# Optimization experiments

Hardware: AMD Instinct MI355X
Metric: run time of the kernel (lower is better)

Reference implementation:

```python
import jax, jax.numpy as jnp
import numpy as np

HEADS = 8
CONTEXT_FRAMES = 128
REL_POS_MAX = 128


def setup_inputs() -> dict:
    key = jax.random.key(0)
    ks = jax.random.split(key, 6)
    b, c, f, t = 2, 512, 64, 512
    x = jax.random.normal(ks[0], (b, c, f, t), dtype=jnp.float32)
    # Linear weights stored as [in, out] (equivalent to torch weight.T)
    W_qkv = jax.random.normal(ks[1], (c, 3 * c), dtype=jnp.float32) * (c ** -0.5)
    b_qkv = jnp.zeros((3 * c,), dtype=jnp.float32)
    W_proj = jax.random.normal(ks[2], (c, c), dtype=jnp.float32) * (c ** -0.5)
    b_proj = jnp.zeros((c,), dtype=jnp.float32)
    rel_pos_bias = jax.random.normal(ks[3], (HEADS, REL_POS_MAX), dtype=jnp.float32) * 0.02
    return {"x": x, "W_qkv": W_qkv, "b_qkv": b_qkv, "W_proj": W_proj,
            "b_proj": b_proj, "rel_pos_bias": rel_pos_bias}


def reference(x, W_qkv, b_qkv, W_proj, b_proj, rel_pos_bias):
    b, c, f, t = x.shape
    hd = c // HEADS
    # (b, c, f, t) -> (b*f, t, c)
    h = jnp.transpose(x, (0, 2, 3, 1)).reshape(b * f, t, c)
    qkv = (h @ W_qkv + b_qkv).reshape(b * f, t, 3, HEADS, hd)
    q, k, v = qkv[:, :, 0], qkv[:, :, 1], qkv[:, :, 2]  # [bf, t, H, hd]
    scale = hd ** -0.5
    scores = jnp.einsum('nqhd,nkhd->nhqk', q, k) * scale  # [bf, H, t, t]
    # causal band mask + gathered relative-position bias
    dist = jnp.arange(t)[:, None] - jnp.arange(t)[None, :]  # [t, t]
    invalid = (dist < 0) | (dist >= CONTEXT_FRAMES)
    bias = rel_pos_bias[:, jnp.clip(dist, 0, REL_POS_MAX - 1)]  # [H, t, t]
    scores = scores + bias[None]
    scores = jnp.where(invalid[None, None], -jnp.inf, scores)
    attn = jax.nn.softmax(scores, axis=-1)
    y = jnp.einsum('nhqk,nkhd->nqhd', attn, v).reshape(b * f, t, c)
    y = y @ W_proj + b_proj
    return jnp.transpose(y.reshape(b, f, t, c), (0, 3, 1, 2))
```

## Files before the change

kernel.cpp:

```cpp
#include <hip/hip_runtime.h>
#include <hip/hip_bf16.h>

typedef short s16x8 __attribute__((ext_vector_type(8)));
typedef unsigned short u16x4 __attribute__((ext_vector_type(4)));
typedef float f32x4 __attribute__((ext_vector_type(4)));

#define MFMA16(a,b,c) __builtin_amdgcn_mfma_f32_16x16x32_bf16((a),(b),(c),0,0,0)

__device__ __forceinline__ unsigned short f2bf(float x){
  unsigned int u = __float_as_uint(x);
  u += 0x7fffu + ((u >> 16) & 1u);
  return (unsigned short)(u >> 16);
}

__device__ __forceinline__ void gl_lds16(const unsigned short* g, unsigned short* l){
  __builtin_amdgcn_global_load_lds((const __attribute__((address_space(1))) unsigned int*)g,
                                   (__attribute__((address_space(3))) unsigned int*)l, 16, 0, 0);
}

__global__ void __launch_bounds__(256) wt_prep(const float* __restrict__ Wq, const float* __restrict__ Wp,
                                               unsigned short* __restrict__ WqT, unsigned short* __restrict__ WpT){
  __shared__ unsigned short tb[64][65];
  int blk = blockIdx.x;
  const float* src; unsigned short* dst; int N, k0, n0;
  if (blk < 192){
    src = Wq; dst = WqT; N = 1536;
    n0 = (blk % 24)*64; k0 = (blk / 24)*64;
  } else {
    blk -= 192; src = Wp; dst = WpT; N = 512;
    n0 = (blk & 7)*64; k0 = (blk >> 3)*64;
  }
  const int tid = threadIdx.x;
  const int nl = tid & 63;
  #pragma unroll
  for (int it = 0; it < 16; ++it){
    const int kl = it*4 + (tid >> 6);
    tb[kl][nl] = f2bf(src[(size_t)(k0+kl)*N + n0 + nl]);
  }
  __syncthreads();
  const int c2 = (tid & 31)*2;
  #pragma unroll
  for (int it = 0; it < 8; ++it){
    const int nw = it*8 + (tid >> 5);
    unsigned int v = (unsigned int)tb[c2][nw] | ((unsigned int)tb[c2+1][nw] << 16);
    *(unsigned int*)(dst + (size_t)(n0+nw)*512 + k0 + c2) = v;
  }
}

__global__ void __launch_bounds__(256) x_to_h(const float* __restrict__ x, unsigned short* __restrict__ h){
  __shared__ unsigned short tb[64][65];
  const int blk = blockIdx.x;
  const int ttt = blk & 7, cht = (blk >> 3) & 7, n = blk >> 6;
  const int b = n >> 6, f = n & 63;
  const int t = threadIdx.x;
  const int tt0 = ttt*64, ch0 = cht*64;
  const float* xb = x + ((size_t)(b*512 + ch0)*64 + f)*512 + tt0;
  const int ttl = t & 63;
  #pragma unroll
  for (int it = 0; it < 16; ++it){
    const int chl = it*4 + (t >> 6);
    tb[chl][ttl] = f2bf(xb[(size_t)chl*32768 + ttl]);
  }
  __syncthreads();
  unsigned short* hb = h + ((size_t)n*512 + tt0)*512 + ch0;
  const int c2 = (t & 31)*2;
  #pragma unroll
  for (int it = 0; it < 8; ++it){
    const int ttw = it*8 + (t >> 5);
    unsigned int v = (unsigned int)tb[c2][ttw] | ((unsigned int)tb[c2+1][ttw] << 16);
    *(unsigned int*)(hb + (size_t)ttw*512 + c2) = v;
  }
}

__device__ __forceinline__ void gemm_core_128(const unsigned short* __restrict__ A,
                                              const unsigned short* __restrict__ Bt,
                                              char* smem, int bm, int bn, int tid,
                                              f32x4 (&acc)[4][4]){
  const int lane = tid & 63, w = tid >> 6;
  const int wr = w >> 1, wc = w & 1;
  const int glog = (lane & 7) ^ ((lane >> 3) & 7);
  const unsigned short* Ab = A  + (size_t)(bm*128 + w*32 + (lane>>3))*512 + glog*8;
  const unsigned short* Bb = Bt + (size_t)(bn*128 + w*32 + (lane>>3))*512 + glog*8;
  unsigned short* AsW = (unsigned short*)smem + w*2048;
  unsigned short* BsW = (unsigned short*)(smem + 16384) + w*2048;
  const int rowoff = (lane & 15)*128;
  const int axor = lane & 7;
  const int ag = lane >> 4;
  for (int kt = 0; kt < 8; ++kt){
    const unsigned short* Ag = Ab + kt*64;
    const unsigned short* Bg = Bb + kt*64;
    gl_lds16(Ag          , AsW);
    gl_lds16(Ag +  8*512 , AsW + 512);
    gl_lds16(Ag + 16*512 , AsW + 1024);
    gl_lds16(Ag + 24*512 , AsW + 1536);
    gl_lds16(Bg          , BsW);
    gl_lds16(Bg +  8*512 , BsW + 512);
    gl_lds16(Bg + 16*512 , BsW + 1024);
    gl_lds16(Bg + 24*512 , BsW + 1536);
    __syncthreads();
    #pragma unroll
    for (int ks = 0; ks < 2; ++ks){
      s16x8 av[4], bv[4];
      const int g16 = ((ks*4 + ag) ^ axor) * 16;
      #pragma unroll
      for (int i = 0; i < 4; ++i){
        av[i] = *(const s16x8*)(smem +         (wr*64 + i*16)*128 + rowoff + g16);
        bv[i] = *(const s16x8*)(smem + 16384 + (wc*64 + i*16)*128 + rowoff + g16);
      }
      #pragma unroll
      for (int i = 0; i < 4; ++i)
        #pragma unroll
        for (int j = 0; j < 4; ++j)
          acc[i][j] = MFMA16(av[i], bv[j], acc[i][j]);
    }
    __syncthreads();
  }
}

__global__ void __launch_bounds__(256) qkv_gemm(const unsigned short* __restrict__ h,
                                                const unsigned short* __restrict__ WqT,
                                                const float* __restrict__ bqkv,
                                                unsigned short* __restrict__ Qb,
                                                unsigned short* __restrict__ Kb,
                                                unsigned short* __restrict__ Vt){
  __shared__ __align__(16) char smem[34816];
  const int tid = threadIdx.x;
  const int bm = blockIdx.x / 12, bn = blockIdx.x % 12;
  f32x4 acc[4][4] = {};
  gemm_core_128(h, WqT, smem, bm, bn, tid, acc);
  const int lane = tid & 63, w = tid >> 6, wr = w >> 1, wc = w & 1;
  const int c0 = bn * 128;
  float bj[4];
  #pragma unroll
  for (int j = 0; j < 4; ++j) bj[j] = bqkv[c0 + wc*64 + j*16 + (lane & 15)];
  unsigned short* Cs = (unsigned short*)smem;
  #pragma unroll
  for (int i = 0; i < 4; ++i)
    #pragma unroll
    for (int j = 0; j < 4; ++j)
      #pragma unroll
      for (int r = 0; r < 4; ++r){
        const int row = wr*64 + i*16 + (lane>>4)*4 + r;
        const int col = wc*64 + j*16 + (lane & 15);
        Cs[row*136 + col] = f2bf(acc[i][j][r] + bj[j]);
      }
  __syncthreads();
  const int n = bm >> 2, tt0 = (bm & 3) * 128;
  const int sel = bn >> 2, cq0 = (bn & 3) * 128;
  if (sel < 2){
    unsigned short* dst = (sel == 0) ? Qb : Kb;
    #pragma unroll
    for (int it = 0; it < 8; ++it){
      const int idx = it*256 + tid;
      const int row = idx >> 4, colc = (idx & 15)*8;
      const int cq = cq0 + colc, head = cq >> 6, d0 = cq & 63;
      s16x8 v = *(const s16x8*)(Cs + row*136 + colc);
      *(s16x8*)(dst + ((size_t)(n*8 + head)*512 + tt0 + row)*64 + d0) = v;
    }
  } else {
    const int col = tid >> 1;
    const int cq = cq0 + col, head = cq >> 6, d = cq & 63;
    #pragma unroll
    for (int it = 0; it < 8; ++it){
      const int ttl0 = (it*2 + (tid & 1))*8;
      s16x8 v;
      #pragma unroll
      for (int r = 0; r < 8; ++r) v[r] = (short)Cs[(ttl0 + r)*136 + col];
      *(s16x8*)(Vt + ((size_t)(n*8 + head)*64 + d)*512 + tt0 + ttl0) = v;
    }
  }
}

__global__ void __launch_bounds__(256) attn_kernel(const unsigned short* __restrict__ Qb,
                                                   const unsigned short* __restrict__ Kb,
                                                   const unsigned short* __restrict__ Vt,
                                                   const float* __restrict__ relb,
                                                   unsigned short* __restrict__ ys){
  __shared__ __align__(16) unsigned short KsL[2][4096];
  __shared__ __align__(16) unsigned short VsL[2][4096];
  __shared__ __align__(16) unsigned short P[4][2][16*72];
  __shared__ float biasS[128];
  const int blk = blockIdx.x;
  const int qt = blk & 3, hh = (blk >> 2) & 7, n = blk >> 5;
  const int tid = threadIdx.x, lane = tid & 63, w = tid >> 6;
  if (tid < 128) biasS[tid] = relb[hh*128 + tid];
  const int q0 = qt * 128;
  const size_t nh = (size_t)(n*8 + hh);
  const unsigned short* Kbase = Kb + nh*32768;
  const unsigned short* Vbase = Vt + nh*32768;
  const int lq = lane & 15, lg = lane >> 4;
  const int qq0 = q0 + w*32;
  s16x8 bq[2][2];
  #pragma unroll
  for (int qs = 0; qs < 2; ++qs){
    const unsigned short* Qp = Qb + (nh*512 + qq0 + qs*16 + lq)*64 + lg*8;
    bq[qs][0] = *(const s16x8*)(Qp);
    bq[qs][1] = *(const s16x8*)(Qp + 32);
  }
  int r_[2], g_[2], dsl_[2];
  #pragma unroll
  for (int j = 0; j < 2; ++j){
    const int slot = j*256 + w*64 + lane;
    r_[j] = slot >> 3;
    g_[j] = (slot & 7) ^ (r_[j] & 7);
    dsl_[j] = (j*256 + w*64) * 8;
  }
  f32x4 yacc[2][4] = {{{0.f,0.f,0.f,0.f}}};
  float m_run[2] = {-INFINITY, -INFINITY}, l_run[2] = {0.f, 0.f};
  const int first = (q0 >= 128) ? 0 : ((128 - q0 + 63) >> 6);
  int cur = 0;
  {
    const int kt0 = q0 - 128 + first*64;
    #pragma unroll
    for (int j = 0; j < 2; ++j){
      gl_lds16(Kbase + (size_t)(kt0 + r_[j])*64 + g_[j]*8, KsL[0] + dsl_[j]);
      gl_lds16(Vbase + (size_t)r_[j]*512 + kt0 + g_[j]*8,  VsL[0] + dsl_[j]);
    }
  }
  for (int kt = first; kt < 4; ++kt){
    const int kt0 = q0 - 128 + kt*64;
    __syncthreads();
    if (kt < 3){
      const int nk0 = kt0 + 64;
      #pragma unroll
      for (int j = 0; j < 2; ++j){
        gl_lds16(Kbase + (size_t)(nk0 + r_[j])*64 + g_[j]*8, KsL[cur^1] + dsl_[j]);
        gl_lds16(Vbase + (size_t)r_[j]*512 + nk0 + g_[j]*8,  VsL[cur^1] + dsl_[j]);
      }
    }
    const bool wact = (kt0 <= qq0 + 31);
    if (wact){
      s16x8 av[4][2];
      #pragma unroll
      for (int mk = 0; mk < 4; ++mk){
        const int rr = mk*16 + lq;
        const unsigned short* kp = KsL[cur] + rr*64;
        av[mk][0] = *(const s16x8*)(kp + ((lg     ) ^ (rr & 7))*8);
        av[mk][1] = *(const s16x8*)(kp + ((4 + lg ) ^ (rr & 7))*8);
      }
      float pex[2][4][4];
      #pragma unroll
      for (int qs = 0; qs < 2; ++qs){
        const int qqs = qq0 + qs*16;
        if (kt0 > qqs + 15 || kt0 + 63 < qqs - 127) continue;
        f32x4 s4[4] = {{0.f,0.f,0.f,0.f}};
        #pragma unroll
        for (int mk = 0; mk < 4; ++mk){
          s4[mk] = MFMA16(av[mk][0], bq[qs][0], s4[mk]);
          s4[mk] = MFMA16(av[mk][1], bq[qs][1], s4[mk]);
        }
        const int qg = qqs + lq;
        float pmax = -3.0e38f;
        #pragma unroll
        for (int mk = 0; mk < 4; ++mk)
          #pragma unroll
          for (int r = 0; r < 4; ++r){
            const int dist = qg - (kt0 + mk*16 + lg*4 + r);
            float xv;
            if (dist >= 0 && dist < 128) xv = s4[mk][r]*0.125f + biasS[dist];
            else                         xv = -1.0e30f;
            pex[qs][mk][r] = xv;
            pmax = fmaxf(pmax, xv);
          }
        pmax = fmaxf(pmax, __shfl_xor(pmax, 16, 64));
        pmax = fmaxf(pmax, __shfl_xor(pmax, 32, 64));
        const float m_new = fmaxf(m_run[qs], pmax);
        const float scalef = __expf(m_run[qs] - m_new);
        float psum = 0.f;
        unsigned short* Pw = P[w][qs];
        #pragma unroll
        for (int mk = 0; mk < 4; ++mk){
          u16x4 pk;
          #pragma unroll
          for (int r = 0; r < 4; ++r){
            const float pe = __expf(pex[qs][mk][r] - m_new);
            psum += pe;
            pk[r] = f2bf(pe);
          }
          *(u16x4*)(Pw + lq*72 + mk*16 + lg*4) = pk;
        }
        psum += __shfl_xor(psum, 16, 64);
        psum += __shfl_xor(psum, 32, 64);
        l_run[qs] = l_run[qs]*scalef + psum;
        m_run[qs] = m_new;
        #pragma unroll
        for (int i = 0; i < 4; ++i) yacc[qs][i] *= scalef;
      }
      s16x8 vv[4][2];
      #pragma unroll
      for (int i = 0; i < 4; ++i){
        const int rr = i*16 + lq;
        const unsigned short* vp = VsL[cur] + rr*64;
        vv[i][0] = *(const s16x8*)(vp + ((lg    ) ^ (rr & 7))*8);
        vv[i][1] = *(const s16x8*)(vp + ((4 + lg) ^ (rr & 7))*8);
      }
      #pragma unroll
      for (int qs = 0; qs < 2; ++qs){
        const int qqs = qq0 + qs*16;
        if (kt0 > qqs + 15 || kt0 + 63 < qqs - 127) continue;
        unsigned short* Pw = P[w][qs];
        #pragma unroll
        for (int ks2 = 0; ks2 < 2; ++ks2){
          s16x8 pb = *(const s16x8*)(Pw + lq*72 + ks2*32 + lg*8);
          #pragma unroll
          for (int i = 0; i < 4; ++i)
            yacc[qs][i] = MFMA16(vv[i][ks2], pb, yacc[qs][i]);
        }
      }
    }
    cur ^= 1;
  }
  #pragma unroll
  for (int qs = 0; qs < 2; ++qs){
    const float inv = 1.f / l_run[qs];
    unsigned short* yp = ys + ((size_t)n*512 + qq0 + qs*16 + lq)*512 + hh*64 + lg*4;
    #pragma unroll
    for (int i = 0; i < 4; ++i){
      u16x4 o;
      #pragma unroll
      for (int r = 0; r < 4; ++r) o[r] = f2bf(yacc[qs][i][r]*inv);
      *(u16x4*)(yp + i*16) = o;
    }
  }
}

__global__ void __launch_bounds__(256) proj_gemm(const unsigned short* __restrict__ ys,
                                                 const unsigned short* __restrict__ WpT,
                                                 const float* __restrict__ bproj,
                                                 float* __restrict__ out){
  __shared__ __align__(16) char smem[34816];
  const int tid = threadIdx.x;
  const int bm = blockIdx.x >> 2, bn = blockIdx.x & 3;
  f32x4 acc[4][4] = {};
  gemm_core_128(ys, WpT, smem, bm, bn, tid, acc);
  const int lane = tid & 63, w = tid >> 6, wr = w >> 1, wc = w & 1;
  const int c0 = bn * 128;
  float bj[4];
  #pragma unroll
  for (int j = 0; j < 4; ++j) bj[j] = bproj[c0 + wc*64 + j*16 + (lane & 15)];
  float* Cs = (float*)smem;
  const int n = bm >> 2, b = n >> 6, f = n & 63, tt0 = (bm & 3)*128;
  #pragma unroll
  for (int p = 0; p < 2; ++p){
    __syncthreads();
    if (wr == p){
      #pragma unroll
      for (int i = 0; i < 4; ++i)
        #pragma unroll
        for (int j = 0; j < 4; ++j)
          #pragma unroll
          for (int r = 0; r < 4; ++r){
            const int rowl = i*16 + (lane>>4)*4 + r;
            const int col = wc*64 + j*16 + (lane & 15);
            Cs[rowl*133 + col] = acc[i][j][r] + bj[j];
          }
    }
    __syncthreads();
    #pragma unroll
    for (int it = 0; it < 8; ++it){
      const int idx = it*256 + tid;
      const int chl = idx >> 4, tc = (idx & 15)*4;
      f32x4 v;
      #pragma unroll
      for (int r = 0; r < 4; ++r) v[r] = Cs[(tc + r)*133 + chl];
      const int ch = c0 + chl;
      *(f32x4*)(out + ((size_t)(b*512 + ch)*64 + f)*512 + tt0 + p*64 + tc) = v;
    }
  }
}

extern "C" void kernel_launch(void* const* d_in, const int* in_sizes, int n_in,
                              void* d_out, int out_size, void* d_ws, size_t ws_size,
                              hipStream_t stream){
  const float* x     = (const float*)d_in[0];
  const float* Wqkv  = (const float*)d_in[1];
  const float* bqkv  = (const float*)d_in[2];
  const float* Wproj = (const float*)d_in[3];
  const float* bproj = (const float*)d_in[4];
  const float* relb  = (const float*)d_in[5];
  float* out = (float*)d_out;
  char* ws = (char*)d_ws;
  if (ws_size < (size_t)270532608) return;
  unsigned short* hbuf = (unsigned short*)(ws);
  unsigned short* Qb   = (unsigned short*)(ws + (size_t)67108864);
  unsigned short* Kb   = (unsigned short*)(ws + (size_t)134217728);
  unsigned short* Vt   = (unsigned short*)(ws + (size_t)201326592);
  unsigned short* WqT  = (unsigned short*)(ws + (size_t)268435456);
  unsigned short* WpT  = (unsigned short*)(ws + (size_t)270008320);

  hipLaunchKernelGGL(wt_prep,     dim3(256),  dim3(256), 0, stream, Wqkv, Wproj, WqT, WpT);
  hipLaunchKernelGGL(x_to_h,      dim3(8192), dim3(256), 0, stream, x, hbuf);
  hipLaunchKernelGGL(qkv_gemm,    dim3(6144), dim3(256), 0, stream, hbuf, WqT, bqkv, Qb, Kb, Vt);
  hipLaunchKernelGGL(attn_kernel, dim3(4096), dim3(256), 0, stream, Qb, Kb, Vt, relb, hbuf);
  hipLaunchKernelGGL(proj_gemm,   dim3(2048), dim3(256), 0, stream, hbuf, WpT, bproj, out);
}
```

Measured before the change: 386.5 us.

## Replace 128x128 GEMMs with double-buffered 256x256 tiles using 8 waves

Both the QKV and projection GEMMs move from a 128x128 tile with 4 waves and single-buffered LDS to a 256x256 tile with 8 waves, 128KB of dynamic LDS and double buffering. The next K-slice's global-to-LDS loads are interleaved with MFMA phases using s_barrier, sched_barrier and setprio. Block indices are remapped in groups of 8 for better L2 locality. The aim is more data reuse per load and overlap of loads with compute, at the cost of fewer blocks, lower occupancy and a more complex epilogue that is split into two halves.

```diff
diff --git a/kernel.cpp b/kernel.cpp
--- a/kernel.cpp
+++ b/kernel.cpp
@@ -72,101 +72,232 @@
   }
 }
 
-__device__ __forceinline__ void gemm_core_128(const unsigned short* __restrict__ A,
+__device__ __forceinline__ void gemm_core_256(const unsigned short* __restrict__ A,
                                               const unsigned short* __restrict__ Bt,
                                               char* smem, int bm, int bn, int tid,
-                                              f32x4 (&acc)[4][4]){
+                                              f32x4 (&acc)[8][4]){
   const int lane = tid & 63, w = tid >> 6;
-  const int wr = w >> 1, wc = w & 1;
-  const int glog = (lane & 7) ^ ((lane >> 3) & 7);
-  const unsigned short* Ab = A  + (size_t)(bm*128 + w*32 + (lane>>3))*512 + glog*8;
-  const unsigned short* Bb = Bt + (size_t)(bn*128 + w*32 + (lane>>3))*512 + glog*8;
-  unsigned short* AsW = (unsigned short*)smem + w*2048;
-  unsigned short* BsW = (unsigned short*)(smem + 16384) + w*2048;
-  const int rowoff = (lane & 15)*128;
-  const int axor = lane & 7;
-  const int ag = lane >> 4;
+  const int wm = w >> 2, wn = w & 3;
+  const int lq = lane & 15, lg = lane >> 4;
+  const unsigned short* Ag[4]; const unsigned short* Bg[4]; int wub[4];
+  #pragma unroll
+  for (int j = 0; j < 4; ++j){
+    const int slot = j*512 + tid;
+    const int srow = slot >> 3;
+    const int sg = (slot & 7) ^ (srow & 7);
+    Ag[j] = A  + (size_t)(bm*256 + srow)*512 + sg*8;
+    Bg[j] = Bt + (size_t)(bn*256 + srow)*512 + sg*8;
+    wub[j] = (j*512 + w*64)*8;
+  }
+  unsigned short* LA[2] = {(unsigned short*)smem,           (unsigned short*)(smem + 65536)};
+  unsigned short* LB[2] = {(unsigned short*)(smem + 32768), (unsigned short*)(smem + 98304)};
+  int raby[8], rbby[4];
+  #pragma unroll
+  for (int i = 0; i < 8; ++i) raby[i] = (wm*128 + i*16 + lq)*128;
+  #pragma unroll
+  for (int j = 0; j < 4; ++j) rbby[j] = (wn*64 + j*16 + lq)*128;
+  const int cg0 = ((lg    ) ^ (lq & 7))*16;
+  const int cg1 = ((4 + lg) ^ (lq & 7))*16;
+  #pragma unroll
+  for (int j = 0; j < 4; ++j){ gl_lds16(Ag[j], LA[0] + wub[j]); gl_lds16(Bg[j], LB[0] + wub[j]); }
+  __syncthreads();
   for (int kt = 0; kt < 8; ++kt){
-    const unsigned short* Ag = Ab + kt*64;
-    const unsigned short* Bg = Bb + kt*64;
-    gl_lds16(Ag          , AsW);
-    gl_lds16(Ag +  8*512 , AsW + 512);
-    gl_lds16(Ag + 16*512 , AsW + 1024);
-    gl_lds16(Ag + 24*512 , AsW + 1536);
-    gl_lds16(Bg          , BsW);
-    gl_lds16(Bg +  8*512 , BsW + 512);
-    gl_lds16(Bg + 16*512 , BsW + 1024);
-    gl_lds16(Bg + 24*512 , BsW + 1536);
-    __syncthreads();
-    #pragma unroll
-    for (int ks = 0; ks < 2; ++ks){
-      s16x8 av[4], bv[4];
-      const int g16 = ((ks*4 + ag) ^ axor) * 16;
-      #pragma unroll
-      for (int i = 0; i < 4; ++i){
-        av[i] = *(const s16x8*)(smem +         (wr*64 + i*16)*128 + rowoff + g16);
-        bv[i] = *(const s16x8*)(smem + 16384 + (wc*64 + i*16)*128 + rowoff + g16);
-      }
-      #pragma unroll
-      for (int i = 0; i < 4; ++i)
+    const int cur = kt & 1;
+    const char* Ab = (const char*)LA[cur];
+    const char* Bb = (const char*)LB[cur];
+    unsigned short* An = LA[cur^1]; unsigned short* Bn = LB[cur^1];
+    const int nko = (kt + 1)*64;
+    const bool st = (kt < 7);
+    s16x8 a[4][2], b0[2][2], b1[2][2];
+    #pragma unroll
+    for (int i = 0; i < 4; ++i){
+      a[i][0] = *(const s16x8*)(Ab + raby[i] + cg0);
+      a[i][1] = *(const s16x8*)(Ab + raby[i] + cg1);
+    }
+    #pragma unroll
+    for (int j = 0; j < 2; ++j){
+      b0[j][0] = *(const s16x8*)(Bb + rbby[j] + cg0);
+      b0[j][1] = *(const s16x8*)(Bb + rbby[j] + cg1);
+    }
+    if (st){ gl_lds16(Ag[0] + nko, An + wub[0]); gl_lds16(Ag[1] + nko, An + wub[1]); }
+    __builtin_amdgcn_sched_barrier(0);
+    __builtin_amdgcn_s_barrier();
+    __builtin_amdgcn_sched_barrier(0);
+    __builtin_amdgcn_s_setprio(1);
+    #pragma unroll
+    for (int i = 0; i < 4; ++i)
+      #pragma unroll
+      for (int j = 0; j < 2; ++j){
+        acc[i][j] = MFMA16(a[i][0], b0[j][0], acc[i][j]);
+        acc[i][j] = MFMA16(a[i][1], b0[j][1], acc[i][j]);
+      }
+    __builtin_amdgcn_s_setprio(0);
+    __builtin_amdgcn_sched_barrier(0);
+    __builtin_amdgcn_s_barrier();
+    __builtin_amdgcn_sched_barrier(0);
+    #pragma unroll
+    for (int j = 0; j < 2; ++j){
+      b1[j][0] = *(const s16x8*)(Bb + rbby[2+j] + cg0);
+      b1[j][1] = *(const s16x8*)(Bb + rbby[2+j] + cg1);
+    }
+    if (st){ gl_lds16(Ag[2] + nko, An + wub[2]); gl_lds16(Ag[3] + nko, An + wub[3]); }
+    __builtin_amdgcn_sched_barrier(0);
+    __builtin_amdgcn_s_barrier();
+    __builtin_amdgcn_sched_barrier(0);
+    __builtin_amdgcn_s_setprio(1);
+    #pragma unroll
+    for (int i = 0; i < 4; ++i)
+      #pragma unroll
+      for (int j = 0; j < 2; ++j){
+        acc[i][2+j] = MFMA16(a[i][0], b1[j][0], acc[i][2+j]);
+        acc[i][2+j] = MFMA16(a[i][1], b1[j][1], acc[i][2+j]);
+      }
+    __builtin_amdgcn_s_setprio(0);
+    __builtin_amdgcn_sched_barrier(0);
+    __builtin_amdgcn_s_barrier();
+    __builtin_amdgcn_sched_barrier(0);
+    #pragma unroll
+    for (int i = 0; i < 4; ++i){
+      a[i][0] = *(const s16x8*)(Ab + raby[4+i] + cg0);
+      a[i][1] = *(const s16x8*)(Ab + raby[4+i] + cg1);
+    }
+    if (st){ gl_lds16(Bg[0] + nko, Bn + wub[0]); gl_lds16(Bg[1] + nko, Bn + wub[1]); }
+    __builtin_amdgcn_sched_barrier(0);
+    __builtin_amdgcn_s_barrier();
+    __builtin_amdgcn_sched_barrier(0);
+    __builtin_amdgcn_s_setprio(1);
+    #pragma unroll
+    for (int i = 0; i < 4; ++i)
+      #pragma unroll
+      for (int j = 0; j < 2; ++j){
+        acc[4+i][j] = MFMA16(a[i][0], b0[j][0], acc[4+i][j]);
+        acc[4+i][j] = MFMA16(a[i][1], b0[j][1], acc[4+i][j]);
+      }
+    __builtin_amdgcn_s_setprio(0);
+    __builtin_amdgcn_sched_barrier(0);
+    __builtin_amdgcn_s_barrier();
+    __builtin_amdgcn_sched_barrier(0);
+    if (st){ gl_lds16(Bg[2] + nko, Bn + wub[2]); gl_lds16(Bg[3] + nko, Bn + wub[3]); }
+    __builtin_amdgcn_sched_barrier(0);
+    __builtin_amdgcn_s_barrier();
+    __builtin_amdgcn_sched_barrier(0);
+    __builtin_amdgcn_s_setprio(1);
+    #pragma unroll
+    for (int i = 0; i < 4; ++i)
+      #pragma unroll
+      for (int j = 0; j < 2; ++j){
+        acc[4+i][2+j] = MFMA16(a[i][0], b1[j][0], acc[4+i][2+j]);
+        acc[4+i][2+j] = MFMA16(a[i][1], b1[j][1], acc[4+i][2+j]);
+      }
+    __builtin_amdgcn_s_setprio(0);
+    __syncthreads();
+  }
+}
+
+__global__ void __launch_bounds__(512, 2) qkv_gemm256(const unsigned short* __restrict__ h,
+                                                      const unsigned short* __restrict__ WqT,
+                                                      const float* __restrict__ bqkv,
+                                                      unsigned short* __restrict__ Qb,
+                                                      unsigned short* __restrict__ Kb,
+                                                      unsigned short* __restrict__ Vt){
+  extern __shared__ __align__(16) char smem[];
+  const int tid = threadIdx.x;
+  const int orig = blockIdx.x;
+  const int wg = (orig & 7)*192 + (orig >> 3);
+  const int bm = wg / 6, bn = wg % 6;
+  f32x4 acc[8][4] = {};
+  gemm_core_256(h, WqT, smem, bm, bn, tid, acc);
+  const int lane = tid & 63, w = tid >> 6;
+  const int wm = w >> 2, wn = w & 3;
+  const int lq = lane & 15, lg = lane >> 4;
+  float bj[4];
+  #pragma unroll
+  for (int j = 0; j < 4; ++j) bj[j] = bqkv[bn*256 + wn*64 + j*16 + lq];
+  const int n = bm >> 1, tt0 = (bm & 1)*256;
+  const int sel = bn >> 1, cq0 = (bn & 1)*256;
+  unsigned short* Cs = (unsigned short*)smem;
+  #pragma unroll
+  for (int mh = 0; mh < 2; ++mh){
+    __syncthreads();
+    if (wm == mh){
+      #pragma unroll
+      for (int i = 0; i < 8; ++i)
         #pragma unroll
         for (int j = 0; j < 4; ++j)
-          acc[i][j] = MFMA16(av[i], bv[j], acc[i][j]);
-    }
-    __syncthreads();
-  }
-}
-
-__global__ void __launch_bounds__(256) qkv_gemm(const unsigned short* __restrict__ h,
-                                                const unsigned short* __restrict__ WqT,
-                                                const float* __restrict__ bqkv,
-                                                unsigned short* __restrict__ Qb,
-                                                unsigned short* __restrict__ Kb,
-                                                unsigned short* __restrict__ Vt){
-  __shared__ __align__(16) char smem[34816];
+          #pragma unroll
+          for (int r = 0; r < 4; ++r)
+            Cs[(i*16 + lg*4 + r)*264 + wn*64 + j*16 + lq] = f2bf(acc[i][j][r] + bj[j]);
+    }
+    __syncthreads();
+    if (sel < 2){
+      unsigned short* dst = (sel == 0) ? Qb : Kb;
+      #pragma unroll
+      for (int it = 0; it < 8; ++it){
+        const int idx = it*512 + tid;
+        const int rowl = idx >> 5, c8 = (idx & 31)*8;
+        const int cq = cq0 + c8, head = cq >> 6, d0 = cq & 63;
+        const int tg = tt0 + mh*128 + rowl;
+        *(s16x8*)(dst + ((size_t)(n*8 + head)*512 + tg)*64 + d0) = *(const s16x8*)(Cs + rowl*264 + c8);
+      }
+    } else {
+      const int col = tid >> 1;
+      const int cq = cq0 + col, head = cq >> 6, d = cq & 63;
+      #pragma unroll
+      for (int seg = 0; seg < 8; ++seg){
+        const int r0 = (tid & 1)*64 + seg*8;
+        s16x8 v;
+        #pragma unroll
+        for (int r = 0; r < 8; ++r) v[r] = (short)Cs[(r0 + r)*264 + col];
+        const int tg0 = tt0 + mh*128 + r0;
+        *(s16x8*)(Vt + ((size_t)(n*8 + head)*64 + d)*512 + tg0) = v;
+      }
+    }
+  }
+}
+
+__global__ void __launch_bounds__(512, 2) proj_gemm256(const unsigned short* __restrict__ ys,
+                                                       const unsigned short* __restrict__ WpT,
+                                                       const float* __restrict__ bproj,
+                                                       float* __restrict__ out){
+  extern __shared__ __align__(16) char smem[];
   const int tid = threadIdx.x;
-  const int bm = blockIdx.x / 12, bn = blockIdx.x % 12;
-  f32x4 acc[4][4] = {};
-  gemm_core_128(h, WqT, smem, bm, bn, tid, acc);
-  const int lane = tid & 63, w = tid >> 6, wr = w >> 1, wc = w & 1;
-  const int c0 = bn * 128;
+  const int orig = blockIdx.x;
+  const int wg = (orig & 7)*64 + (orig >> 3);
+  const int bm = wg >> 1, bn = wg & 1;
+  f32x4 acc[8][4] = {};
+  gemm_core_256(ys, WpT, smem, bm, bn, tid, acc);
+  const int lane = tid & 63, w = tid >> 6;
+  const int wm = w >> 2, wn = w & 3;
+  const int lq = lane & 15, lg = lane >> 4;
   float bj[4];
   #pragma unroll
-  for (int j = 0; j < 4; ++j) bj[j] = bqkv[c0 + wc*64 + j*16 + (lane & 15)];
-  unsigned short* Cs = (unsigned short*)smem;
-  #pragma unroll
-  for (int i = 0; i < 4; ++i)
-    #pragma unroll
-    for (int j = 0; j < 4; ++j)
-      #pragma unroll
-      for (int r = 0; r < 4; ++r){
-        const int row = wr*64 + i*16 + (lane>>4)*4 + r;
-        const int col = wc*64 + j*16 + (lane & 15);
-        Cs[row*136 + col] = f2bf(acc[i][j][r] + bj[j]);
-      }
-  __syncthreads();
-  const int n = bm >> 2, tt0 = (bm & 3) * 128;
-  const int sel = bn >> 2, cq0 = (bn & 3) * 128;
-  if (sel < 2){
-    unsigned short* dst = (sel == 0) ? Qb : Kb;
-    #pragma unroll
-    for (int it = 0; it < 8; ++it){
-      const int idx = it*256 + tid;
-      const int row = idx >> 4, colc = (idx & 15)*8;
-      const int cq = cq0 + colc, head = cq >> 6, d0 = cq & 63;
-      s16x8 v = *(const s16x8*)(Cs + row*136 + colc);
-      *(s16x8*)(dst + ((size_t)(n*8 + head)*512 + tt0 + row)*64 + d0) = v;
-    }
-  } else {
-    const int col = tid >> 1;
-    const int cq = cq0 + col, head = cq >> 6, d = cq & 63;
-    #pragma unroll
-    for (int it = 0; it < 8; ++it){
-      const int ttl0 = (it*2 + (tid & 1))*8;
-      s16x8 v;
-      #pragma unroll
-      for (int r = 0; r < 8; ++r) v[r] = (short)Cs[(ttl0 + r)*136 + col];
-      *(s16x8*)(Vt + ((size_t)(n*8 + head)*64 + d)*512 + tt0 + ttl0) = v;
+  for (int j = 0; j < 4; ++j) bj[j] = bproj[bn*256 + wn*64 + j*16 + lq];
+  const int n = bm >> 1, tt0 = (bm & 1)*256;
+  const int b = n >> 6, f = n & 63;
+  float* Csf = (float*)smem;
+  #pragma unroll
+  for (int mh = 0; mh < 2; ++mh){
+    __syncthreads();
+    if (wm == mh){
+      #pragma unroll
+      for (int i = 0; i < 8; ++i)
+        #pragma unroll
+        for (int j = 0; j < 4; ++j)
+          #pragma unroll
+          for (int r = 0; r < 4; ++r)
+            Csf[(i*16 + lg*4 + r)*256 + wn*64 + j*16 + lq] = acc[i][j][r] + bj[j];
+    }
+    __syncthreads();
+    const int ch = tid >> 1;
+    const int chg = bn*256 + ch;
+    #pragma unroll
+    for (int s = 0; s < 16; ++s){
+      const int r0 = (tid & 1)*64 + s*4;
+      f32x4 v;
+      #pragma unroll
+      for (int r = 0; r < 4; ++r) v[r] = Csf[(r0 + r)*256 + ch];
+      const int tg = tt0 + mh*128 + r0;
+      *(f32x4*)(out + ((size_t)(b*512 + chg)*64 + f)*512 + tg) = v;
     }
   }
 }
@@ -324,51 +455,6 @@
   }
 }
 
-__global__ void __launch_bounds__(256) proj_gemm(const unsigned short* __restrict__ ys,
-                                                 const unsigned short* __restrict__ WpT,
-                                                 const float* __restrict__ bproj,
-                                                 float* __restrict__ out){
-  __shared__ __align__(16) char smem[34816];
-  const int tid = threadIdx.x;
-  const int bm = blockIdx.x >> 2, bn = blockIdx.x & 3;
-  f32x4 acc[4][4] = {};
-  gemm_core_128(ys, WpT, smem, bm, bn, tid, acc);
-  const int lane = tid & 63, w = tid >> 6, wr = w >> 1, wc = w & 1;
-  const int c0 = bn * 128;
-  float bj[4];
-  #pragma unroll
-  for (int j = 0; j < 4; ++j) bj[j] = bproj[c0 + wc*64 + j*16 + (lane & 15)];
-  float* Cs = (float*)smem;
-  const int n = bm >> 2, b = n >> 6, f = n & 63, tt0 = (bm & 3)*128;
-  #pragma unroll
-  for (int p = 0; p < 2; ++p){
-    __syncthreads();
-    if (wr == p){
-      #pragma unroll
-      for (int i = 0; i < 4; ++i)
-        #pragma unroll
-        for (int j = 0; j < 4; ++j)
-          #pragma unroll
-          for (int r = 0; r < 4; ++r){
-            const int rowl = i*16 + (lane>>4)*4 + r;
-            const int col = wc*64 + j*16 + (lane & 15);
-            Cs[rowl*133 + col] = acc[i][j][r] + bj[j];
-          }
-    }
-    __syncthreads();
-    #pragma unroll
-    for (int it = 0; it < 8; ++it){
-      const int idx = it*256 + tid;
-      const int chl = idx >> 4, tc = (idx & 15)*4;
-      f32x4 v;
-      #pragma unroll
-      for (int r = 0; r < 4; ++r) v[r] = Cs[(tc + r)*133 + chl];
-      const int ch = c0 + chl;
-      *(f32x4*)(out + ((size_t)(b*512 + ch)*64 + f)*512 + tt0 + p*64 + tc) = v;
-    }
-  }
-}
-
 extern "C" void kernel_launch(void* const* d_in, const int* in_sizes, int n_in,
                               void* d_out, int out_size, void* d_ws, size_t ws_size,
                               hipStream_t stream){
@@ -388,9 +474,14 @@
   unsigned short* WqT  = (unsigned short*)(ws + (size_t)268435456);
   unsigned short* WpT  = (unsigned short*)(ws + (size_t)270008320);
 
-  hipLaunchKernelGGL(wt_prep,     dim3(256),  dim3(256), 0, stream, Wqkv, Wproj, WqT, WpT);
-  hipLaunchKernelGGL(x_to_h,      dim3(8192), dim3(256), 0, stream, x, hbuf);
-  hipLaunchKernelGGL(qkv_gemm,    dim3(6144), dim3(256), 0, stream, hbuf, WqT, bqkv, Qb, Kb, Vt);
-  hipLaunchKernelGGL(attn_kernel, dim3(4096), dim3(256), 0, stream, Qb, Kb, Vt, relb, hbuf);
-  hipLaunchKernelGGL(proj_gemm,   dim3(2048), dim3(256), 0, stream, hbuf, WpT, bproj, out);
-}
+  hipFuncSetAttribute(reinterpret_cast<const void*>(qkv_gemm256),
+                      hipFuncAttributeMaxDynamicSharedMemorySize, 131072);
+  hipFuncSetAttribute(reinterpret_cast<const void*>(proj_gemm256),
+                      hipFuncAttributeMaxDynamicSharedMemorySize, 131072);
+
+  hipLaunchKernelGGL(wt_prep,      dim3(256),  dim3(256), 0, stream, Wqkv, Wproj, WqT, WpT);
+  hipLaunchKernelGGL(x_to_h,       dim3(8192), dim3(256), 0, stream, x, hbuf);
+  hipLaunchKernelGGL(qkv_gemm256,  dim3(1536), dim3(512), 131072, stream, hbuf, WqT, bqkv, Qb, Kb, Vt);
+  hipLaunchKernelGGL(attn_kernel,  dim3(4096), dim3(256), 0, stream, Qb, Kb, Vt, relb, hbuf);
+  hipLaunchKernelGGL(proj_gemm256, dim3(512),  dim3(512), 131072, stream, hbuf, WpT, bproj, out);
+}
```

Measured after the change: 395.1 us. +2.2%, slower.
